# Kernel optimization log

Hardware: AMD Instinct MI355X
Metric: run time of the kernel (lower is better)

Reference implementation:

```python
import jax, jax.numpy as jnp
import numpy as np

BN_EPS = 1e-5

# Binary activation with hardtanh STE semantics (forward: sign)
@jax.custom_vjp
def binary_act(x):
    return jnp.sign(x)

def _ba_fwd(x):
    return jnp.sign(x), x

def _ba_bwd(x, g):
    return (jnp.where(jnp.abs(x) > 1.0, 0.0, g),)

binary_act.defvjp(_ba_fwd, _ba_bwd)

# Binary weight quantizer (forward: sign, backward: identity STE)
@jax.custom_vjp
def binary_w(x):
    return jnp.sign(x)

def _bw_fwd(x):
    return jnp.sign(x), None

def _bw_bwd(_, g):
    return (g,)

binary_w.defvjp(_bw_fwd, _bw_bwd)


def setup_inputs() -> dict:
    key = jax.random.key(0)
    k1, k2, k3 = jax.random.split(key, 3)
    B, C_in, H, W_sp = 32, 256, 56, 56
    C_out, KH, KW = 256, 3, 3
    x = jax.random.normal(k1, (B, C_in, H, W_sp), dtype=jnp.float32)
    weight = jax.random.normal(k2, (C_out, C_in, KH, KW), dtype=jnp.float32) * 0.05
    bias = jax.random.normal(k3, (C_out,), dtype=jnp.float32) * 0.01
    gamma = jnp.ones((C_out,), dtype=jnp.float32)
    beta = jnp.zeros((C_out,), dtype=jnp.float32)
    return {"x": x, "weight": weight, "bias": bias, "gamma": gamma, "beta": beta}


def reference(x, weight, bias, gamma, beta):
    # --- activation binarization (A=2): sign ---
    xb = binary_act(x)
    # --- weight binarization (W=2): mean-center over in-channel dim, clamp, sign * alpha ---
    wc = weight - jnp.mean(weight, axis=1, keepdims=True)
    wc = jnp.clip(wc, -1.0, 1.0)
    alpha = jnp.mean(jnp.abs(wc), axis=(1, 2, 3), keepdims=True)  # per-output-channel scale
    wq = binary_w(wc) * alpha
    # --- conv2d, stride 1, padding 1 ---
    y = jax.lax.conv_general_dilated(
        xb, wq, window_strides=(1, 1), padding=((1, 1), (1, 1)),
        dimension_numbers=("NCHW", "OIHW", "NCHW"))
    y = y + bias[None, :, None, None]
    # --- BatchNorm2d (training-mode batch statistics, biased variance) ---
    mu = jnp.mean(y, axis=(0, 2, 3), keepdims=True)
    var = jnp.var(y, axis=(0, 2, 3), keepdims=True)
    y = (y - mu) * jax.lax.rsqrt(var + BN_EPS)
    y = y * gamma[None, :, None, None] + beta[None, :, None, None]
    # --- last_relu=1 ---
    y = jax.nn.relu(y)
    # --- last_bin=1 (A=2 -> binary activation) ---
    y = binary_act(y)
    return y
```

## Files before the change

### kernel.cpp

```cpp
#include <hip/hip_runtime.h>

typedef unsigned long long u64;
typedef int i32x4 __attribute__((ext_vector_type(4)));
typedef int i32x16 __attribute__((ext_vector_type(16)));
typedef short s16x8 __attribute__((ext_vector_type(8)));

#define N_SP 3136
#define C_IN 256
#define C_OUT 256
#define BATCH 32
#define NBLK 896
#define XROW 64
#define XPLANE (58 * XROW * 256)
#define XSIZE ((size_t)BATCH * XPLANE)
#define S16_OFF ((size_t)36 << 20)
#define S16_BYTES ((size_t)BATCH * C_OUT * N_SP * 2)

__global__ __launch_bounds__(256) void prep_weights(const float* __restrict__ w,
                                                    char* __restrict__ A_pack,
                                                    double* __restrict__ alpha) {
    const int o = blockIdx.x;
    const int i = threadIdx.x;
    const int lane = i & 63, wvid = i >> 6;
    __shared__ double part[4][9];
    __shared__ double part2[4];

    float wv[9];
    const float* wp = w + ((size_t)o * C_IN + i) * 9;
#pragma unroll
    for (int t = 0; t < 9; ++t) wv[t] = wp[t];

#pragma unroll
    for (int t = 0; t < 9; ++t) {
        double v = (double)wv[t];
#pragma unroll
        for (int off = 32; off > 0; off >>= 1) v += __shfl_down(v, off);
        if (lane == 0) part[wvid][t] = v;
    }
    __syncthreads();

    double asum = 0.0;
#pragma unroll
    for (int t = 0; t < 9; ++t) {
        double mean = (part[0][t] + part[1][t] + part[2][t] + part[3][t]) * (1.0 / 256.0);
        double wc = (double)wv[t] - mean;
        int idx16 = ((t * 8 + (i >> 5)) * 8 + (o >> 5)) * 64 + (((i >> 4) & 1) << 5) + (o & 31);
        A_pack[(size_t)idx16 * 16 + (i & 15)] = (char)(wc > 0.0 ? 1 : -1);
        double aw = fabs(wc);
        if (aw > 1.0) aw = 1.0;
        asum += aw;
    }
#pragma unroll
    for (int off = 32; off > 0; off >>= 1) asum += __shfl_down(asum, off);
    if (lane == 0) part2[wvid] = asum;
    __syncthreads();
    if (i == 0)
        alpha[o] = (part2[0] + part2[1] + part2[2] + part2[3]) * (1.0 / 2304.0);
}

__global__ __launch_bounds__(256) void sign_transpose(const float* __restrict__ x,
                                                      char* __restrict__ xsT) {
    const int sp0 = blockIdx.x * 64;
    const int b = blockIdx.y;
    const int lane = threadIdx.x & 63;
    const int wv = threadIdx.x >> 6;
    __shared__ char tile[64 * 272];

    {
        const int tidl = (blockIdx.y * 49 + blockIdx.x) * 256 + threadIdx.x;
        if (tidl < 294912) {
            const int bb = tidl / 9216;
            const int r = tidl - bb * 9216;
            int hp, wp, c16;
            if (r < 2048) {
                hp = (r >> 10) * 57;
                wp = (r >> 4) & 63;
                c16 = (r & 15) << 4;
            } else {
                int r2 = r - 2048;
                hp = 1 + (r2 >> 7);
                int q = r2 & 127;
                int wi = q >> 4;
                wp = (wi == 0) ? 0 : 56 + wi;
                c16 = (q & 15) << 4;
            }
            *(i32x4*)(xsT + (((size_t)(bb * 58 + hp) << 6) + wp) * 256 + c16) =
                (i32x4){0, 0, 0, 0};
        }
    }

    const float* xp = x + ((size_t)(b * 256 + (wv << 6))) * N_SP + sp0 + lane;
#pragma unroll
    for (int q = 0; q < 4; ++q) {
        unsigned d[4];
#pragma unroll
        for (int dd = 0; dd < 4; ++dd) {
            unsigned v = 0;
#pragma unroll
            for (int kk = 0; kk < 4; ++kk) {
                int ci_l = (q << 4) + (dd << 2) + kk;
                float xv = xp[(size_t)ci_l * N_SP];
                v |= (unsigned)(xv > 0.0f ? 0x01u : 0xFFu) << (8 * kk);
            }
            d[dd] = v;
        }
        *(i32x4*)(tile + lane * 272 + (wv << 6) + (q << 4)) =
            (i32x4){(int)d[0], (int)d[1], (int)d[2], (int)d[3]};
    }
    __syncthreads();

    const int t = threadIdx.x;
#pragma unroll
    for (int j = 0; j < 4; ++j) {
        int sp_loc = (j << 4) + (t >> 4);
        int ci0 = (t & 15) << 4;
        i32x4 v = *(const i32x4*)(tile + sp_loc * 272 + ci0);
        int spg = sp0 + sp_loc;
        int h = spg / 56, w = spg - h * 56;
        size_t dst = (((size_t)(b * 58 + h + 1) << 6) + (w + 1)) * 256 + ci0;
        *(i32x4*)(xsT + dst) = v;
    }
}

__global__ __launch_bounds__(256, 1) void conv_mfma(const char* __restrict__ xsT,
                                                    const char* __restrict__ A_pack,
                                                    float* __restrict__ out,
                                                    short* __restrict__ s16,
                                                    int2* __restrict__ partials) {
    const int tid = threadIdx.x;
    const int lane = tid & 63;
    const int wv = tid >> 6;
    const int l31 = lane & 31, l5 = lane >> 5;
    const int blk = blockIdx.x;
    const int b = blk / 28;
    const int h0 = (blk - b * 28) * 2;

    __shared__ char slab[4 * 58 * 272];

    {
        const char* src = xsT + ((size_t)(b * 58 + h0) << 6) * 256;
        for (int c = tid; c < 4 * 58 * 16; c += 256) {
            int dh = c / (58 * 16);
            int rem = c - dh * (58 * 16);
            int wp = rem >> 4, c16 = (rem & 15) << 4;
            *(i32x4*)(slab + (dh * 58 + wp) * 272 + c16) =
                *(const i32x4*)(src + (size_t)dh * (XROW * 256) + wp * 256 + c16);
        }
    }
    __syncthreads();

    i32x16 acc[2][2][2] = {};

    const char* apb = A_pack + ((size_t)(2 * wv * 64 + lane)) * 16;
    const char* sb0 = slab + l31 * 272 + l5 * 16;
    int w1_0 = 32 + l31;     if (w1_0 > 57) w1_0 = 57;
    int w1_1 = 33 + l31;     if (w1_1 > 57) w1_1 = 57;
    int w1_2 = 34 + l31;     if (w1_2 > 57) w1_2 = 57;
    const char* sb1_0 = slab + w1_0 * 272 + l5 * 16;
    const char* sb1_1 = slab + w1_1 * 272 + l5 * 16;
    const char* sb1_2 = slab + w1_2 * 272 + l5 * 16;

#pragma unroll
    for (int tap = 0; tap < 9; ++tap) {
        const int dh = tap / 3, dw = tap - 3 * (tap / 3);
        const char* sb1 = (dw == 0) ? sb1_0 : ((dw == 1) ? sb1_1 : sb1_2);
#pragma unroll
        for (int cib = 0; cib < 8; ++cib) {
            const int it = tap * 8 + cib;
            i32x4 a0 = *(const i32x4*)(apb + (size_t)it * 8192);
            i32x4 a1 = *(const i32x4*)(apb + (size_t)it * 8192 + 1024);
            i32x4 b00 = *(const i32x4*)(sb0 + ((dh + 0) * 58 + dw) * 272 + cib * 32);
            i32x4 b01 = *(const i32x4*)(sb0 + ((dh + 1) * 58 + dw) * 272 + cib * 32);
            i32x4 b10 = *(const i32x4*)(sb1 + (dh + 0) * 58 * 272 + cib * 32);
            i32x4 b11 = *(const i32x4*)(sb1 + (dh + 1) * 58 * 272 + cib * 32);
            acc[0][0][0] = __builtin_amdgcn_mfma_i32_32x32x32_i8(a0, b00, acc[0][0][0], 0, 0, 0);
            acc[0][0][1] = __builtin_amdgcn_mfma_i32_32x32x32_i8(a0, b01, acc[0][0][1], 0, 0, 0);
            acc[0][1][0] = __builtin_amdgcn_mfma_i32_32x32x32_i8(a0, b10, acc[0][1][0], 0, 0, 0);
            acc[0][1][1] = __builtin_amdgcn_mfma_i32_32x32x32_i8(a0, b11, acc[0][1][1], 0, 0, 0);
            acc[1][0][0] = __builtin_amdgcn_mfma_i32_32x32x32_i8(a1, b00, acc[1][0][0], 0, 0, 0);
            acc[1][0][1] = __builtin_amdgcn_mfma_i32_32x32x32_i8(a1, b01, acc[1][0][1], 0, 0, 0);
            acc[1][1][0] = __builtin_amdgcn_mfma_i32_32x32x32_i8(a1, b10, acc[1][1][0], 0, 0, 0);
            acc[1][1][1] = __builtin_amdgcn_mfma_i32_32x32x32_i8(a1, b11, acc[1][1][1], 0, 0, 0);
        }
    }

    if (s16) {
        short* sb = s16 + ((size_t)(b * 256)) * N_SP + h0 * 56;
#pragma unroll
        for (int co_i = 0; co_i < 2; ++co_i) {
            const int co5 = 2 * wv + co_i;
#pragma unroll
            for (int nh = 0; nh < 2; ++nh) {
                const int w = nh * 32 + l31;
                if (w < 56) {
#pragma unroll
                    for (int row = 0; row < 2; ++row)
#pragma unroll
                        for (int reg = 0; reg < 16; ++reg) {
                            int corow = (reg & 3) + 8 * (reg >> 2) + 4 * l5;
                            sb[(size_t)(co5 * 32 + corow) * N_SP + row * 56 + w] =
                                (short)acc[co_i][nh][row][reg];
                        }
                }
            }
        }
    } else {
        float* ob = out + ((size_t)(b * 256)) * N_SP + h0 * 56;
#pragma unroll
        for (int co_i = 0; co_i < 2; ++co_i) {
            const int co5 = 2 * wv + co_i;
#pragma unroll
            for (int nh = 0; nh < 2; ++nh) {
                const int w = nh * 32 + l31;
                if (w < 56) {
#pragma unroll
                    for (int row = 0; row < 2; ++row)
#pragma unroll
                        for (int reg = 0; reg < 16; ++reg) {
                            int corow = (reg & 3) + 8 * (reg >> 2) + 4 * l5;
                            ob[(size_t)(co5 * 32 + corow) * N_SP + row * 56 + w] =
                                (float)acc[co_i][nh][row][reg];
                        }
                }
            }
        }
    }

    __syncthreads();
    int* sp_s = (int*)slab;
    int* sp_q = (int*)slab + 256;
#pragma unroll
    for (int co_i = 0; co_i < 2; ++co_i) {
#pragma unroll
        for (int reg = 0; reg < 16; ++reg) {
            int v00 = acc[co_i][0][0][reg], v01 = acc[co_i][0][1][reg];
            int v10 = (l31 < 24) ? acc[co_i][1][0][reg] : 0;
            int v11 = (l31 < 24) ? acc[co_i][1][1][reg] : 0;
            int s = v00 + v01 + v10 + v11;
            unsigned q = (unsigned)(v00 * v00) + (unsigned)(v01 * v01)
                       + (unsigned)(v10 * v10) + (unsigned)(v11 * v11);
#pragma unroll
            for (int off = 16; off > 0; off >>= 1) {
                s += __shfl_xor(s, off);
                q += (unsigned)__shfl_xor((int)q, off);
            }
            if (l31 == 0) {
                int corow = (reg & 3) + 8 * (reg >> 2) + 4 * l5;
                sp_s[(2 * wv + co_i) * 32 + corow] = s;
                sp_q[(2 * wv + co_i) * 32 + corow] = (int)q;
            }
        }
    }
    __syncthreads();
    partials[(size_t)tid * NBLK + blk] = make_int2(sp_s[tid], sp_q[tid]);
}

__global__ __launch_bounds__(256) void stats_consts(const int2* __restrict__ partials,
                                                    const double* __restrict__ alpha,
                                                    const float* __restrict__ gamma,
                                                    const float* __restrict__ beta,
                                                    double* __restrict__ AB) {
    const int c = blockIdx.x;
    const int t = threadIdx.x;
    long long s1 = 0, s2 = 0;
    for (int blk = t; blk < NBLK; blk += 256) {
        int2 v = partials[(size_t)c * NBLK + blk];
        s1 += v.x;
        s2 += (long long)v.y;
    }
#pragma unroll
    for (int off = 32; off > 0; off >>= 1) {
        s1 += __shfl_down(s1, off);
        s2 += __shfl_down(s2, off);
    }
    __shared__ long long p1[4], p2[4];
    if ((t & 63) == 0) { p1[t >> 6] = s1; p2[t >> 6] = s2; }
    __syncthreads();
    if (t == 0) {
        double S1 = (double)(p1[0] + p1[1] + p1[2] + p1[3]);
        double S2 = (double)(p2[0] + p2[1] + p2[2] + p2[3]);
        const double N = (double)(BATCH * N_SP);
        double mu = S1 / N;
        double var = S2 / N - mu * mu;
        double a = alpha[c];
        double vy = a * a * var;
        double scale = (double)gamma[c] / sqrt(vy + 1e-5);
        double A = a * scale;
        double B = (double)beta[c] - A * mu;
        AB[c] = A;
        AB[C_OUT + c] = B;
    }
}

__global__ __launch_bounds__(256) void finalize(float* __restrict__ out,
                                                const double* __restrict__ AB) {
    const unsigned i4 = blockIdx.x * 256 + threadIdx.x;
    const unsigned e = i4 << 2;
    const int c = (int)((e / N_SP) & (C_OUT - 1));
    const double A = AB[c];
    const double B = AB[C_OUT + c];
    float4 v = ((float4*)out)[i4];
    v.x = (A * (double)v.x + B) > 0.0 ? 1.0f : 0.0f;
    v.y = (A * (double)v.y + B) > 0.0 ? 1.0f : 0.0f;
    v.z = (A * (double)v.z + B) > 0.0 ? 1.0f : 0.0f;
    v.w = (A * (double)v.w + B) > 0.0 ? 1.0f : 0.0f;
    ((float4*)out)[i4] = v;
}

__global__ __launch_bounds__(256) void finalize16(const short* __restrict__ S,
                                                  float* __restrict__ out,
                                                  const double* __restrict__ AB) {
    const unsigned t = blockIdx.x * 256 + threadIdx.x;
    const unsigned e = t << 3;
    const int c = (int)((e / N_SP) & (C_OUT - 1));
    const double A = AB[c];
    const double B = AB[C_OUT + c];
    s16x8 v = *(const s16x8*)(S + e);
    float4 o0, o1;
    o0.x = (A * (double)v[0] + B) > 0.0 ? 1.0f : 0.0f;
    o0.y = (A * (double)v[1] + B) > 0.0 ? 1.0f : 0.0f;
    o0.z = (A * (double)v[2] + B) > 0.0 ? 1.0f : 0.0f;
    o0.w = (A * (double)v[3] + B) > 0.0 ? 1.0f : 0.0f;
    o1.x = (A * (double)v[4] + B) > 0.0 ? 1.0f : 0.0f;
    o1.y = (A * (double)v[5] + B) > 0.0 ? 1.0f : 0.0f;
    o1.z = (A * (double)v[6] + B) > 0.0 ? 1.0f : 0.0f;
    o1.w = (A * (double)v[7] + B) > 0.0 ? 1.0f : 0.0f;
    *(float4*)(out + e) = o0;
    *(float4*)(out + e + 4) = o1;
}

extern "C" void kernel_launch(void* const* d_in, const int* in_sizes, int n_in,
                              void* d_out, int out_size, void* d_ws, size_t ws_size,
                              hipStream_t stream) {
    const float* x      = (const float*)d_in[0];
    const float* weight = (const float*)d_in[1];
    const float* bias   = (const float*)d_in[2];   (void)bias;
    const float* gamma  = (const float*)d_in[3];
    const float* beta   = (const float*)d_in[4];
    float* out = (float*)d_out;

    char* ws = (char*)d_ws;
    double* alpha = (double*)(ws + 4096);
    double* AB    = (double*)(ws + 8192);
    char*   A_pack = (char*)(ws + 16384);
    int2*   partials = (int2*)(ws + (1 << 20));
    char*   xsT   = (char*)(ws + (5 << 20));
    const bool use16 = ws_size >= S16_OFF + S16_BYTES;
    short*  s16 = use16 ? (short*)(ws + S16_OFF) : (short*)0;

    prep_weights<<<C_OUT, 256, 0, stream>>>(weight, A_pack, alpha);
    sign_transpose<<<dim3(49, BATCH), 256, 0, stream>>>(x, xsT);
    conv_mfma<<<dim3(NBLK), 256, 0, stream>>>(xsT, A_pack, out, s16, partials);
    stats_consts<<<C_OUT, 256, 0, stream>>>(partials, alpha, gamma, beta, AB);
    if (use16)
        finalize16<<<12544, 256, 0, stream>>>(s16, out, AB);
    else
        finalize<<<(out_size / 4) / 256, 256, 0, stream>>>(out, AB);
}
```

Baseline: 361.3 us.

## Halve conv tile height for higher occupancy and add nontemporal memory hints

The conv kernel now computes one output row per block instead of two. That doubles the block count, shrinks the LDS slab and accumulator registers, and raises the launch-bounds occupancy target to 3 blocks per CU. Separately, nontemporal loads and stores are applied to the streaming input pack, the conv output, the partials and the finalize pass to reduce cache pollution. The cost is more halo reloading and twice as many weight fragment loads per MFMA, since each A fragment is now reused across two B tiles instead of four.

```diff
diff --git a/kernel.cpp b/kernel.cpp
--- a/kernel.cpp
+++ b/kernel.cpp
@@ -4,12 +4,13 @@
 typedef int i32x4 __attribute__((ext_vector_type(4)));
 typedef int i32x16 __attribute__((ext_vector_type(16)));
 typedef short s16x8 __attribute__((ext_vector_type(8)));
+typedef float f32x4 __attribute__((ext_vector_type(4)));
 
 #define N_SP 3136
 #define C_IN 256
 #define C_OUT 256
 #define BATCH 32
-#define NBLK 896
+#define NBLK 1792
 #define XROW 64
 #define XPLANE (58 * XROW * 256)
 #define XSIZE ((size_t)BATCH * XPLANE)
@@ -99,7 +100,7 @@
 #pragma unroll
             for (int kk = 0; kk < 4; ++kk) {
                 int ci_l = (q << 4) + (dd << 2) + kk;
-                float xv = xp[(size_t)ci_l * N_SP];
+                float xv = __builtin_nontemporal_load(xp + (size_t)ci_l * N_SP);
                 v |= (unsigned)(xv > 0.0f ? 0x01u : 0xFFu) << (8 * kk);
             }
             d[dd] = v;
@@ -122,7 +123,7 @@
     }
 }
 
-__global__ __launch_bounds__(256, 1) void conv_mfma(const char* __restrict__ xsT,
+__global__ __launch_bounds__(256, 3) void conv_mfma(const char* __restrict__ xsT,
                                                     const char* __restrict__ A_pack,
                                                     float* __restrict__ out,
                                                     short* __restrict__ s16,
@@ -132,14 +133,14 @@
     const int wv = tid >> 6;
     const int l31 = lane & 31, l5 = lane >> 5;
     const int blk = blockIdx.x;
-    const int b = blk / 28;
-    const int h0 = (blk - b * 28) * 2;
-
-    __shared__ char slab[4 * 58 * 272];
+    const int b = blk / 56;
+    const int h0 = blk - b * 56;
+
+    __shared__ char slab[3 * 58 * 272];
 
     {
         const char* src = xsT + ((size_t)(b * 58 + h0) << 6) * 256;
-        for (int c = tid; c < 4 * 58 * 16; c += 256) {
+        for (int c = tid; c < 3 * 58 * 16; c += 256) {
             int dh = c / (58 * 16);
             int rem = c - dh * (58 * 16);
             int wp = rem >> 4, c16 = (rem & 15) << 4;
@@ -149,7 +150,7 @@
     }
     __syncthreads();
 
-    i32x16 acc[2][2][2] = {};
+    i32x16 acc[2][2] = {};
 
     const char* apb = A_pack + ((size_t)(2 * wv * 64 + lane)) * 16;
     const char* sb0 = slab + l31 * 272 + l5 * 16;
@@ -169,18 +170,12 @@
             const int it = tap * 8 + cib;
             i32x4 a0 = *(const i32x4*)(apb + (size_t)it * 8192);
             i32x4 a1 = *(const i32x4*)(apb + (size_t)it * 8192 + 1024);
-            i32x4 b00 = *(const i32x4*)(sb0 + ((dh + 0) * 58 + dw) * 272 + cib * 32);
-            i32x4 b01 = *(const i32x4*)(sb0 + ((dh + 1) * 58 + dw) * 272 + cib * 32);
-            i32x4 b10 = *(const i32x4*)(sb1 + (dh + 0) * 58 * 272 + cib * 32);
-            i32x4 b11 = *(const i32x4*)(sb1 + (dh + 1) * 58 * 272 + cib * 32);
-            acc[0][0][0] = __builtin_amdgcn_mfma_i32_32x32x32_i8(a0, b00, acc[0][0][0], 0, 0, 0);
-            acc[0][0][1] = __builtin_amdgcn_mfma_i32_32x32x32_i8(a0, b01, acc[0][0][1], 0, 0, 0);
-            acc[0][1][0] = __builtin_amdgcn_mfma_i32_32x32x32_i8(a0, b10, acc[0][1][0], 0, 0, 0);
-            acc[0][1][1] = __builtin_amdgcn_mfma_i32_32x32x32_i8(a0, b11, acc[0][1][1], 0, 0, 0);
-            acc[1][0][0] = __builtin_amdgcn_mfma_i32_32x32x32_i8(a1, b00, acc[1][0][0], 0, 0, 0);
-            acc[1][0][1] = __builtin_amdgcn_mfma_i32_32x32x32_i8(a1, b01, acc[1][0][1], 0, 0, 0);
-            acc[1][1][0] = __builtin_amdgcn_mfma_i32_32x32x32_i8(a1, b10, acc[1][1][0], 0, 0, 0);
-            acc[1][1][1] = __builtin_amdgcn_mfma_i32_32x32x32_i8(a1, b11, acc[1][1][1], 0, 0, 0);
+            i32x4 b0 = *(const i32x4*)(sb0 + (dh * 58 + dw) * 272 + cib * 32);
+            i32x4 b1 = *(const i32x4*)(sb1 + dh * 58 * 272 + cib * 32);
+            acc[0][0] = __builtin_amdgcn_mfma_i32_32x32x32_i8(a0, b0, acc[0][0], 0, 0, 0);
+            acc[0][1] = __builtin_amdgcn_mfma_i32_32x32x32_i8(a0, b1, acc[0][1], 0, 0, 0);
+            acc[1][0] = __builtin_amdgcn_mfma_i32_32x32x32_i8(a1, b0, acc[1][0], 0, 0, 0);
+            acc[1][1] = __builtin_amdgcn_mfma_i32_32x32x32_i8(a1, b1, acc[1][1], 0, 0, 0);
         }
     }
 
@@ -194,13 +189,12 @@
                 const int w = nh * 32 + l31;
                 if (w < 56) {
 #pragma unroll
-                    for (int row = 0; row < 2; ++row)
-#pragma unroll
-                        for (int reg = 0; reg < 16; ++reg) {
-                            int corow = (reg & 3) + 8 * (reg >> 2) + 4 * l5;
-                            sb[(size_t)(co5 * 32 + corow) * N_SP + row * 56 + w] =
-                                (short)acc[co_i][nh][row][reg];
-                        }
+                    for (int reg = 0; reg < 16; ++reg) {
+                        int corow = (reg & 3) + 8 * (reg >> 2) + 4 * l5;
+                        __builtin_nontemporal_store(
+                            (short)acc[co_i][nh][reg],
+                            sb + (size_t)(co5 * 32 + corow) * N_SP + w);
+                    }
                 }
             }
         }
@@ -214,13 +208,12 @@
                 const int w = nh * 32 + l31;
                 if (w < 56) {
 #pragma unroll
-                    for (int row = 0; row < 2; ++row)
-#pragma unroll
-                        for (int reg = 0; reg < 16; ++reg) {
-                            int corow = (reg & 3) + 8 * (reg >> 2) + 4 * l5;
-                            ob[(size_t)(co5 * 32 + corow) * N_SP + row * 56 + w] =
-                                (float)acc[co_i][nh][row][reg];
-                        }
+                    for (int reg = 0; reg < 16; ++reg) {
+                        int corow = (reg & 3) + 8 * (reg >> 2) + 4 * l5;
+                        __builtin_nontemporal_store(
+                            (float)acc[co_i][nh][reg],
+                            ob + (size_t)(co5 * 32 + corow) * N_SP + w);
+                    }
                 }
             }
         }
@@ -233,12 +226,10 @@
     for (int co_i = 0; co_i < 2; ++co_i) {
 #pragma unroll
         for (int reg = 0; reg < 16; ++reg) {
-            int v00 = acc[co_i][0][0][reg], v01 = acc[co_i][0][1][reg];
-            int v10 = (l31 < 24) ? acc[co_i][1][0][reg] : 0;
-            int v11 = (l31 < 24) ? acc[co_i][1][1][reg] : 0;
-            int s = v00 + v01 + v10 + v11;
-            unsigned q = (unsigned)(v00 * v00) + (unsigned)(v01 * v01)
-                       + (unsigned)(v10 * v10) + (unsigned)(v11 * v11);
+            int v0 = acc[co_i][0][reg];
+            int v1 = (l31 < 24) ? acc[co_i][1][reg] : 0;
+            int s = v0 + v1;
+            unsigned q = (unsigned)(v0 * v0) + (unsigned)(v1 * v1);
 #pragma unroll
             for (int off = 16; off > 0; off >>= 1) {
                 s += __shfl_xor(s, off);
@@ -252,7 +243,10 @@
         }
     }
     __syncthreads();
-    partials[(size_t)tid * NBLK + blk] = make_int2(sp_s[tid], sp_q[tid]);
+    {
+        u64 v = (u64)(unsigned)sp_s[tid] | ((u64)(unsigned)sp_q[tid] << 32);
+        __builtin_nontemporal_store(v, (u64*)(partials + (size_t)tid * NBLK + blk));
+    }
 }
 
 __global__ __launch_bounds__(256) void stats_consts(const int2* __restrict__ partials,
@@ -315,8 +309,8 @@
     const int c = (int)((e / N_SP) & (C_OUT - 1));
     const double A = AB[c];
     const double B = AB[C_OUT + c];
-    s16x8 v = *(const s16x8*)(S + e);
-    float4 o0, o1;
+    s16x8 v = __builtin_nontemporal_load((const s16x8*)(S + e));
+    f32x4 o0, o1;
     o0.x = (A * (double)v[0] + B) > 0.0 ? 1.0f : 0.0f;
     o0.y = (A * (double)v[1] + B) > 0.0 ? 1.0f : 0.0f;
     o0.z = (A * (double)v[2] + B) > 0.0 ? 1.0f : 0.0f;
@@ -325,8 +319,8 @@
     o1.y = (A * (double)v[5] + B) > 0.0 ? 1.0f : 0.0f;
     o1.z = (A * (double)v[6] + B) > 0.0 ? 1.0f : 0.0f;
     o1.w = (A * (double)v[7] + B) > 0.0 ? 1.0f : 0.0f;
-    *(float4*)(out + e) = o0;
-    *(float4*)(out + e + 4) = o1;
+    __builtin_nontemporal_store(o0, (f32x4*)(out + e));
+    __builtin_nontemporal_store(o1, (f32x4*)(out + e + 4));
 }
 
 extern "C" void kernel_launch(void* const* d_in, const int* in_sizes, int n_in,
```

After: 319.0 us. 1.13x faster.
